# Performance work log

Measured on AMD Instinct MI355X. Metric: run time of the kernel, lower is better.

The kernel has to match this reference:

```python
import jax, jax.numpy as jnp
import numpy as np


def _row_forward(rows, W1, b1, W_ih, W_hh, b_ih, b_hh, W3, b3):
    """Batched version of the per-row pipeline: fc1 -> ReLU -> 1-step LSTM (zero init
    state) -> ReLU -> fc3 -> softmax. rows: [N, input_size]."""
    h1 = jax.nn.relu(rows @ W1.T + b1)              # [N, 256]
    # LSTM single step with h0 = c0 = 0: the W_hh @ h0 term vanishes.
    gates = h1 @ W_ih.T + (b_ih + b_hh)             # [N, 4*H2], gate order i,f,g,o
    i, f, g, o = jnp.split(gates, 4, axis=-1)
    c = jax.nn.sigmoid(i) * jnp.tanh(g)             # c = i*g since c0 = 0 (f gate unused)
    h = jax.nn.sigmoid(o) * jnp.tanh(c)             # [N, H2]
    h = jax.nn.relu(h)
    return jax.nn.softmax(h @ W3.T + b3, axis=-1)   # [N, num_classes]


def setup_inputs() -> dict:
    key = jax.random.key(0)
    ks = jax.random.split(key, 9)
    P, M, A, B = 64, 16, 512, 128       # patients, mats/patient, input_size, rows/mat
    H1, H2, C = 256, 256, 32            # hidden1 (hardcoded 256 in view), hidden2, classes
    def w(k, shape, fan):
        return (jax.random.normal(k, shape, jnp.float32) / np.float32(np.sqrt(fan)))
    return {
        "x": jax.random.normal(ks[0], (P, M, A, B), jnp.float32),
        "W1": w(ks[1], (H1, A), A), "b1": w(ks[2], (H1,), A),
        "W_ih": w(ks[3], (4 * H2, H1), H1), "W_hh": w(ks[4], (4 * H2, H2), H2),
        "b_ih": w(ks[5], (4 * H2,), H1), "b_hh": w(ks[6], (4 * H2,), H1),
        "W3": w(ks[7], (C, H2), H2), "b3": w(ks[8], (C,), H2),
    }


def reference(x, W1, b1, W_ih, W_hh, b_ih, b_hh, W3, b3):
    P, M, A, B = x.shape
    # Original iterates rows of mat.transpose(1,0) (i.e. columns of mat). Every row is
    # an independent evaluation because the LSTM hidden state is reset (None) per row,
    # so we batch all P*M*B rows into one fused pipeline.
    rows = x.transpose(0, 1, 3, 2).reshape(P * M * B, A)
    outs = _row_forward(rows, W1, b1, W_ih, W_hh, b_ih, b_hh, W3, b3)  # [P*M*B, C]
    outs = outs.reshape(P, M * B, -1)
    # cumOut keeps only the result of the LAST row of the LAST mat per patient.
    return outs[:, -1, :]  # [P, num_classes]
```

## Files before the change

kernel.cpp:

```cpp
#include <hip/hip_runtime.h>
#include <cmath>

#define NP 64
#define NM 16
#define NA 512
#define NB 128
#define H1 256
#define H2 256
#define NC 32

__device__ __forceinline__ float sigmoid_(float x) {
    return 1.0f / (1.0f + __expf(-x));
}

__device__ __forceinline__ float dot4(float4 a, float4 b, float acc) {
    acc = fmaf(a.x, b.x, acc);
    acc = fmaf(a.y, b.y, acc);
    acc = fmaf(a.z, b.z, acc);
    acc = fmaf(a.w, b.w, acc);
    return acc;
}

extern "C" __global__ __launch_bounds__(256)
void k1_fc1(const float* __restrict__ x,
            const float* __restrict__ W1, const float* __restrict__ b1,
            float* __restrict__ h1out)
{
    __shared__ float rows[8][NA];

    const int pt = blockIdx.x >> 3;
    const int ot = blockIdx.x & 7;
    const int t  = threadIdx.x;

    for (int idx = t; idx < 8 * NA; idx += 256) {
        const int pl = idx >> 9;
        const int a  = idx & (NA - 1);
        const size_t gi = ((((size_t)(pt * 8 + pl) * NM + (NM - 1)) * NA + a) * NB) + (NB - 1);
        rows[pl][a] = x[gi];
    }
    __syncthreads();

    const int pl = t >> 5;
    const int ol = t & 31;
    const int o  = ot * 32 + ol;

    const float4* w = (const float4*)(W1 + (size_t)o * NA);
    const float4* r = (const float4*)rows[pl];

    float a0 = 0.f, a1 = 0.f, a2 = 0.f, a3 = 0.f;
    #pragma unroll 8
    for (int k = 0; k < NA / 4; k += 4) {
        a0 = dot4(w[k + 0], r[k + 0], a0);
        a1 = dot4(w[k + 1], r[k + 1], a1);
        a2 = dot4(w[k + 2], r[k + 2], a2);
        a3 = dot4(w[k + 3], r[k + 3], a3);
    }
    const float v = (a0 + a1) + (a2 + a3) + b1[o];
    h1out[(size_t)(pt * 8 + pl) * H1 + o] = fmaxf(v, 0.f);
}

extern "C" __global__ __launch_bounds__(256)
void k2_lstm(const float* __restrict__ h1in,
             const float* __restrict__ W_ih,
             const float* __restrict__ b_ih, const float* __restrict__ b_hh,
             float* __restrict__ hout)
{
    const int t = threadIdx.x;
    const int j = blockIdx.x * 4 + (t >> 6);
    const int p = t & 63;

    const float4* wi = (const float4*)(W_ih + (size_t)j * H1);
    const float4* wg = (const float4*)(W_ih + (size_t)(2 * H2 + j) * H1);
    const float4* wo = (const float4*)(W_ih + (size_t)(3 * H2 + j) * H1);
    const float4* hv = (const float4*)(h1in + (size_t)p * H1);

    float i0 = 0.f, i1 = 0.f, g0 = 0.f, g1 = 0.f, o0 = 0.f, o1 = 0.f;
    #pragma unroll 8
    for (int k = 0; k < H1 / 4; k += 2) {
        float4 h4a = hv[k], h4b = hv[k + 1];
        i0 = dot4(wi[k], h4a, i0);  i1 = dot4(wi[k + 1], h4b, i1);
        g0 = dot4(wg[k], h4a, g0);  g1 = dot4(wg[k + 1], h4b, g1);
        o0 = dot4(wo[k], h4a, o0);  o1 = dot4(wo[k + 1], h4b, o1);
    }
    const float ai = i0 + i1 + b_ih[j]            + b_hh[j];
    const float ag = g0 + g1 + b_ih[2 * H2 + j]   + b_hh[2 * H2 + j];
    const float ao = o0 + o1 + b_ih[3 * H2 + j]   + b_hh[3 * H2 + j];

    const float c = sigmoid_(ai) * tanhf(ag);
    const float h = sigmoid_(ao) * tanhf(c);
    hout[(size_t)p * H2 + j] = fmaxf(h, 0.f);
}

extern "C" __global__ __launch_bounds__(256)
void k3_fc3(const float* __restrict__ hin,
            const float* __restrict__ W3, const float* __restrict__ b3,
            float* __restrict__ out)
{
    __shared__ float logits[NC];

    const int p = blockIdx.x;
    const int t = threadIdx.x;

    const int g = t >> 3;
    const int l = t & 7;

    const float4* w  = (const float4*)(W3 + (size_t)g * H2);
    const float4* hv = (const float4*)(hin + (size_t)p * H2);
    float acc = 0.f;
    #pragma unroll
    for (int j = 0; j < 8; ++j)
        acc = dot4(w[l + 8 * j], hv[l + 8 * j], acc);

    acc += __shfl_down(acc, 4, 64);
    acc += __shfl_down(acc, 2, 64);
    acc += __shfl_down(acc, 1, 64);
    if (l == 0) logits[g] = acc + b3[g];
    __syncthreads();

    if (t < NC) {
        float v = logits[t];
        float m = v;
        #pragma unroll
        for (int off = 16; off; off >>= 1) m = fmaxf(m, __shfl_xor(m, off, 64));
        float e = __expf(v - m);
        float s = e;
        #pragma unroll
        for (int off = 16; off; off >>= 1) s += __shfl_xor(s, off, 64);
        out[p * NC + t] = e / s;
    }
}

extern "C" void kernel_launch(void* const* d_in, const int* in_sizes, int n_in,
                              void* d_out, int out_size, void* d_ws, size_t ws_size,
                              hipStream_t stream) {
    const float* x    = (const float*)d_in[0];
    const float* W1   = (const float*)d_in[1];
    const float* b1   = (const float*)d_in[2];
    const float* W_ih = (const float*)d_in[3];
    const float* b_ih = (const float*)d_in[5];
    const float* b_hh = (const float*)d_in[6];
    const float* W3   = (const float*)d_in[7];
    const float* b3   = (const float*)d_in[8];
    float* out = (float*)d_out;

    float* h1 = (float*)d_ws;
    float* h  = h1 + (size_t)NP * H1;

    hipLaunchKernelGGL(k1_fc1, dim3(64), dim3(256), 0, stream, x, W1, b1, h1);
    hipLaunchKernelGGL(k2_lstm, dim3(64), dim3(256), 0, stream, h1, W_ih, b_ih, b_hh, h);
    hipLaunchKernelGGL(k3_fc3, dim3(64), dim3(256), 0, stream, h, W3, b3, out);
}
```

Measured before the change: 43.88 us.

## Fuse three stage kernels into one cooperative kernel with grid syncs

Merges the fc1, LSTM-step and fc3+softmax kernels into a single cooperative launch of 64 blocks, using grid-wide syncs between stages in place of separate kernel launches. This targets launch overhead and the gaps between the three dependent small kernels. Cooperative launch and grid.sync carry their own cost, and intermediate results still pass through global memory.

```diff
diff --git a/kernel.cpp b/kernel.cpp
--- a/kernel.cpp
+++ b/kernel.cpp
@@ -1,5 +1,8 @@
 #include <hip/hip_runtime.h>
+#include <hip/hip_cooperative_groups.h>
 #include <cmath>
+
+namespace cg = cooperative_groups;
 
 #define NP 64
 #define NM 16
@@ -22,111 +25,105 @@
 }
 
 extern "C" __global__ __launch_bounds__(256)
-void k1_fc1(const float* __restrict__ x,
-            const float* __restrict__ W1, const float* __restrict__ b1,
-            float* __restrict__ h1out)
+void rnn_coop(const float* __restrict__ x,
+              const float* __restrict__ W1, const float* __restrict__ b1,
+              const float* __restrict__ W_ih,
+              const float* __restrict__ b_ih, const float* __restrict__ b_hh,
+              const float* __restrict__ W3, const float* __restrict__ b3,
+              float* __restrict__ h1ws, float* __restrict__ hws,
+              float* __restrict__ out)
 {
+    cg::grid_group grid = cg::this_grid();
+    const int t = threadIdx.x;
+    const int b = blockIdx.x;
+
     __shared__ float rows[8][NA];
-
-    const int pt = blockIdx.x >> 3;
-    const int ot = blockIdx.x & 7;
-    const int t  = threadIdx.x;
-
-    for (int idx = t; idx < 8 * NA; idx += 256) {
-        const int pl = idx >> 9;
-        const int a  = idx & (NA - 1);
-        const size_t gi = ((((size_t)(pt * 8 + pl) * NM + (NM - 1)) * NA + a) * NB) + (NB - 1);
-        rows[pl][a] = x[gi];
-    }
-    __syncthreads();
-
-    const int pl = t >> 5;
-    const int ol = t & 31;
-    const int o  = ot * 32 + ol;
-
-    const float4* w = (const float4*)(W1 + (size_t)o * NA);
-    const float4* r = (const float4*)rows[pl];
-
-    float a0 = 0.f, a1 = 0.f, a2 = 0.f, a3 = 0.f;
-    #pragma unroll 8
-    for (int k = 0; k < NA / 4; k += 4) {
-        a0 = dot4(w[k + 0], r[k + 0], a0);
-        a1 = dot4(w[k + 1], r[k + 1], a1);
-        a2 = dot4(w[k + 2], r[k + 2], a2);
-        a3 = dot4(w[k + 3], r[k + 3], a3);
-    }
-    const float v = (a0 + a1) + (a2 + a3) + b1[o];
-    h1out[(size_t)(pt * 8 + pl) * H1 + o] = fmaxf(v, 0.f);
-}
-
-extern "C" __global__ __launch_bounds__(256)
-void k2_lstm(const float* __restrict__ h1in,
-             const float* __restrict__ W_ih,
-             const float* __restrict__ b_ih, const float* __restrict__ b_hh,
-             float* __restrict__ hout)
-{
-    const int t = threadIdx.x;
-    const int j = blockIdx.x * 4 + (t >> 6);
-    const int p = t & 63;
-
-    const float4* wi = (const float4*)(W_ih + (size_t)j * H1);
-    const float4* wg = (const float4*)(W_ih + (size_t)(2 * H2 + j) * H1);
-    const float4* wo = (const float4*)(W_ih + (size_t)(3 * H2 + j) * H1);
-    const float4* hv = (const float4*)(h1in + (size_t)p * H1);
-
-    float i0 = 0.f, i1 = 0.f, g0 = 0.f, g1 = 0.f, o0 = 0.f, o1 = 0.f;
-    #pragma unroll 8
-    for (int k = 0; k < H1 / 4; k += 2) {
-        float4 h4a = hv[k], h4b = hv[k + 1];
-        i0 = dot4(wi[k], h4a, i0);  i1 = dot4(wi[k + 1], h4b, i1);
-        g0 = dot4(wg[k], h4a, g0);  g1 = dot4(wg[k + 1], h4b, g1);
-        o0 = dot4(wo[k], h4a, o0);  o1 = dot4(wo[k + 1], h4b, o1);
-    }
-    const float ai = i0 + i1 + b_ih[j]            + b_hh[j];
-    const float ag = g0 + g1 + b_ih[2 * H2 + j]   + b_hh[2 * H2 + j];
-    const float ao = o0 + o1 + b_ih[3 * H2 + j]   + b_hh[3 * H2 + j];
-
-    const float c = sigmoid_(ai) * tanhf(ag);
-    const float h = sigmoid_(ao) * tanhf(c);
-    hout[(size_t)p * H2 + j] = fmaxf(h, 0.f);
-}
-
-extern "C" __global__ __launch_bounds__(256)
-void k3_fc3(const float* __restrict__ hin,
-            const float* __restrict__ W3, const float* __restrict__ b3,
-            float* __restrict__ out)
-{
     __shared__ float logits[NC];
 
-    const int p = blockIdx.x;
-    const int t = threadIdx.x;
+    {
+        const int pt = b >> 3;
+        const int ot = b & 7;
+        for (int idx = t; idx < 8 * NA; idx += 256) {
+            const int pl = idx >> 9;
+            const int a  = idx & (NA - 1);
+            const size_t gi = ((((size_t)(pt * 8 + pl) * NM + (NM - 1)) * NA + a) * NB) + (NB - 1);
+            rows[pl][a] = x[gi];
+        }
+        __syncthreads();
 
-    const int g = t >> 3;
-    const int l = t & 7;
+        const int pl = t >> 5;
+        const int ol = t & 31;
+        const int o  = ot * 32 + ol;
 
-    const float4* w  = (const float4*)(W3 + (size_t)g * H2);
-    const float4* hv = (const float4*)(hin + (size_t)p * H2);
-    float acc = 0.f;
-    #pragma unroll
-    for (int j = 0; j < 8; ++j)
-        acc = dot4(w[l + 8 * j], hv[l + 8 * j], acc);
+        const float4* w = (const float4*)(W1 + (size_t)o * NA);
+        const float4* r = (const float4*)rows[pl];
+        float a0 = 0.f, a1 = 0.f, a2 = 0.f, a3 = 0.f;
+        #pragma unroll 8
+        for (int k = 0; k < NA / 4; k += 4) {
+            a0 = dot4(w[k + 0], r[k + 0], a0);
+            a1 = dot4(w[k + 1], r[k + 1], a1);
+            a2 = dot4(w[k + 2], r[k + 2], a2);
+            a3 = dot4(w[k + 3], r[k + 3], a3);
+        }
+        h1ws[(size_t)(pt * 8 + pl) * H1 + o] =
+            fmaxf((a0 + a1) + (a2 + a3) + b1[o], 0.f);
+    }
+    grid.sync();
 
-    acc += __shfl_down(acc, 4, 64);
-    acc += __shfl_down(acc, 2, 64);
-    acc += __shfl_down(acc, 1, 64);
-    if (l == 0) logits[g] = acc + b3[g];
-    __syncthreads();
+    {
+        const int j = b * 4 + (t >> 6);
+        const int p = t & 63;
 
-    if (t < NC) {
-        float v = logits[t];
-        float m = v;
+        const float4* wi = (const float4*)(W_ih + (size_t)j * H1);
+        const float4* wg = (const float4*)(W_ih + (size_t)(2 * H2 + j) * H1);
+        const float4* wo = (const float4*)(W_ih + (size_t)(3 * H2 + j) * H1);
+        const float4* hv = (const float4*)(h1ws + (size_t)p * H1);
+
+        float i0 = 0.f, i1 = 0.f, g0 = 0.f, g1 = 0.f, o0 = 0.f, o1 = 0.f;
+        #pragma unroll 8
+        for (int k = 0; k < H1 / 4; k += 2) {
+            float4 h4a = hv[k], h4b = hv[k + 1];
+            i0 = dot4(wi[k], h4a, i0);  i1 = dot4(wi[k + 1], h4b, i1);
+            g0 = dot4(wg[k], h4a, g0);  g1 = dot4(wg[k + 1], h4b, g1);
+            o0 = dot4(wo[k], h4a, o0);  o1 = dot4(wo[k + 1], h4b, o1);
+        }
+        const float ai = i0 + i1 + b_ih[j]            + b_hh[j];
+        const float ag = g0 + g1 + b_ih[2 * H2 + j]   + b_hh[2 * H2 + j];
+        const float ao = o0 + o1 + b_ih[3 * H2 + j]   + b_hh[3 * H2 + j];
+        const float c = sigmoid_(ai) * tanhf(ag);
+        const float h = sigmoid_(ao) * tanhf(c);
+        hws[(size_t)p * H2 + j] = fmaxf(h, 0.f);
+    }
+    grid.sync();
+
+    {
+        const int p = b;
+        const int g = t >> 3;
+        const int l = t & 7;
+
+        const float4* w  = (const float4*)(W3 + (size_t)g * H2);
+        const float4* hv = (const float4*)(hws + (size_t)p * H2);
+        float acc = 0.f;
         #pragma unroll
-        for (int off = 16; off; off >>= 1) m = fmaxf(m, __shfl_xor(m, off, 64));
-        float e = __expf(v - m);
-        float s = e;
-        #pragma unroll
-        for (int off = 16; off; off >>= 1) s += __shfl_xor(s, off, 64);
-        out[p * NC + t] = e / s;
+        for (int j = 0; j < 8; ++j)
+            acc = dot4(w[l + 8 * j], hv[l + 8 * j], acc);
+        acc += __shfl_down(acc, 4, 64);
+        acc += __shfl_down(acc, 2, 64);
+        acc += __shfl_down(acc, 1, 64);
+        if (l == 0) logits[g] = acc + b3[g];
+        __syncthreads();
+
+        if (t < NC) {
+            float v = logits[t];
+            float m = v;
+            #pragma unroll
+            for (int off = 16; off; off >>= 1) m = fmaxf(m, __shfl_xor(m, off, 64));
+            float e = __expf(v - m);
+            float s = e;
+            #pragma unroll
+            for (int off = 16; off; off >>= 1) s += __shfl_xor(s, off, 64);
+            out[p * NC + t] = e / s;
+        }
     }
 }
 
@@ -146,7 +143,11 @@
     float* h1 = (float*)d_ws;
     float* h  = h1 + (size_t)NP * H1;
 
-    hipLaunchKernelGGL(k1_fc1, dim3(64), dim3(256), 0, stream, x, W1, b1, h1);
-    hipLaunchKernelGGL(k2_lstm, dim3(64), dim3(256), 0, stream, h1, W_ih, b_ih, b_hh, h);
-    hipLaunchKernelGGL(k3_fc3, dim3(64), dim3(256), 0, stream, h, W3, b3, out);
+    void* args[] = {
+        (void*)&x, (void*)&W1, (void*)&b1, (void*)&W_ih,
+        (void*)&b_ih, (void*)&b_hh, (void*)&W3, (void*)&b3,
+        (void*)&h1, (void*)&h, (void*)&out
+    };
+    hipLaunchCooperativeKernel((const void*)rnn_coop, dim3(NP), dim3(256),
+                               args, 0, stream);
 }
```

Measured after the change: 79.93 us. 82.1% more time.
